# Kernel tuning notes

Hardware: AMD Instinct MI355X
Metric: run time of the kernel (lower is better)

Reference implementation:

```python
import jax, jax.numpy as jnp
import numpy as np

B, S, D, DEPTH = 2, 2048, 1024, 4
NUM_LEAVES = 2 ** DEPTH          # 16
NUM_DEC = NUM_LEAVES - 1         # 15


def setup_inputs() -> dict:
    key = jax.random.key(0)
    k1, k2, k3, k4, k5 = jax.random.split(key, 5)
    scale = 1.0 / np.sqrt(D)
    return {
        "x": jax.random.normal(k1, (B, S, D), dtype=jnp.float32),
        "dec_w": jax.random.normal(k2, (NUM_DEC, D), dtype=jnp.float32) * scale,
        "dec_b": jax.random.normal(k3, (NUM_DEC,), dtype=jnp.float32) * scale,
        "leaf_w": jax.random.normal(k4, (NUM_LEAVES, D, D), dtype=jnp.float32) * scale,  # [leaf, out, in] (torch Linear layout)
        "leaf_b": jax.random.normal(k5, (NUM_LEAVES, D), dtype=jnp.float32) * scale,
    }


def reference(x, dec_w, dec_b, leaf_w, leaf_b):
    num_leaves = leaf_w.shape[0]
    num_dec = num_leaves - 1
    # All decision-node sigmoids in one batched GEMM: [B,S,num_dec]
    dec = jax.nn.sigmoid(jnp.einsum("bsd,nd->bsn", x, dec_w) + dec_b)
    # Faithful to the original: each tree slot is multiplied exactly once by its
    # direct parent's decision (left child: p, right child: 1-p).
    leaf_idx = np.arange(num_dec, 2 * num_leaves - 1)      # slots holding leaf probs
    parent = (leaf_idx - 1) // 2                           # [num_leaves]
    is_left = (leaf_idx % 2 == 1)                          # [num_leaves]
    dec_p = dec[..., parent]                               # [B,S,num_leaves]
    leaf_probs = jnp.where(jnp.asarray(is_left), dec_p, 1.0 - dec_p)
    # All leaf MLPs as one batched GEMM: [B,S,L,D]
    leaf_out = jnp.einsum("bsd,lod->bslo", x, leaf_w) + leaf_b
    # Probability-weighted sum over leaves -> [B,S,D]
    return jnp.einsum("bslo,bsl->bso", leaf_out, leaf_probs)
```

## Files before the change

### kernel.cpp

```cpp
#include <hip/hip_runtime.h>
#include <stdint.h>


#define M_TOK 4096
#define DDIM  1024
#define KFLAT 9216

typedef __bf16 bf16x8 __attribute__((ext_vector_type(8)));
typedef float  f32x4  __attribute__((ext_vector_type(4)));
typedef unsigned short u16x4 __attribute__((ext_vector_type(4)));
typedef unsigned short u16x8 __attribute__((ext_vector_type(8)));

#define GLB(p) ((const __attribute__((address_space(1))) void*)(p))
#define LDS(p) ((__attribute__((address_space(3))) void*)(p))

__device__ __forceinline__ unsigned short f2bf(float f) {
    union { float f; uint32_t u; } v; v.f = f;
    uint32_t u = v.u;
    return (unsigned short)((u + 0x7fffu + ((u >> 16) & 1u)) >> 16);
}

__device__ __forceinline__ bf16x8 asbf(f32x4 v) {
    bf16x8 r; __builtin_memcpy(&r, &v, 16); return r;
}

template<int OFF>
__device__ __forceinline__ f32x4 dsr(uint32_t a) {
    f32x4 r;
    asm volatile("ds_read_b128 %0, %1 offset:%c2" : "=v"(r) : "v"(a), "i"(OFF));
    return r;
}

__global__ __launch_bounds__(256) void prep_dec_kernel(
    const float* __restrict__ x, const float* __restrict__ dec_w,
    const float* __restrict__ dec_b, const float* __restrict__ lw,
    const float* __restrict__ lb, unsigned short* __restrict__ wp,
    float* __restrict__ bw, unsigned short* __restrict__ xs,
    float* __restrict__ pmat, int newlay)
{
    if (blockIdx.x < 1024) {
        int idx = blockIdx.x * 256 + threadIdx.x;
        int o  = idx >> 8;
        int k4 = (idx & 255) << 2;
        size_t src = (size_t)o * DDIM + k4;
        const int nt = o >> 8, wn = (o >> 6) & 3, jj = (o >> 4) & 3, ra = o & 15;
        auto store4 = [&](int l, u16x4 d) {
            if (newlay) {
                int K    = l * DDIM + k4;
                int kt   = K >> 6;
                int half = (K >> 5) & 1;
                int g16  = (K >> 3) & 3;
                int e0   = K & 7;
                size_t a = ((size_t)(nt * 144 + kt) * 4 + wn) * 4096
                         + (jj * 2 + half) * 512 + (g16 * 16 + ra) * 8 + e0;
                *(u16x4*)(wp + a) = d;
            } else {
                *(u16x4*)(wp + (size_t)o * KFLAT + l * DDIM + k4) = d;
            }
        };
        float4 acc = make_float4(0.f, 0.f, 0.f, 0.f);
#pragma unroll
        for (int j = 0; j < 8; ++j) {
            const float4 a = *(const float4*)(lw + (size_t)(2*j)   * DDIM*DDIM + src);
            const float4 b = *(const float4*)(lw + (size_t)(2*j+1) * DDIM*DDIM + src);
            u16x4 d;
            d[0] = f2bf(a.x - b.x); d[1] = f2bf(a.y - b.y);
            d[2] = f2bf(a.z - b.z); d[3] = f2bf(a.w - b.w);
            store4(j, d);
            acc.x += b.x; acc.y += b.y; acc.z += b.z; acc.w += b.w;
        }
        u16x4 s;
        s[0] = f2bf(acc.x); s[1] = f2bf(acc.y); s[2] = f2bf(acc.z); s[3] = f2bf(acc.w);
        store4(8, s);
        if ((idx & 255) == 0) {
            float sb = 0.f;
#pragma unroll
            for (int j = 0; j < 8; ++j) {
                float ba = lb[(2*j) * DDIM + o];
                float bb = lb[(2*j+1) * DDIM + o];
                bw[j * DDIM + o] = ba - bb;
                sb += bb;
            }
            bw[8 * DDIM + o] = sb;
        }
    } else {
        int m    = (blockIdx.x - 1024) * 4 + (threadIdx.x >> 6);
        int lane = threadIdx.x & 63;
        const float* xr = x + (size_t)m * DDIM + lane * 16;
        float xv[16];
        *(float4*)&xv[0]  = *(const float4*)(xr + 0);
        *(float4*)&xv[4]  = *(const float4*)(xr + 4);
        *(float4*)&xv[8]  = *(const float4*)(xr + 8);
        *(float4*)&xv[12] = *(const float4*)(xr + 12);
        float s[8];
#pragma unroll
        for (int j = 0; j < 8; ++j) {
            const float* wr = dec_w + (size_t)(7 + j) * DDIM + lane * 16;
            float a = 0.f;
#pragma unroll
            for (int i = 0; i < 16; i += 4) {
                float4 wv = *(const float4*)(wr + i);
                a = fmaf(xv[i], wv.x, fmaf(xv[i+1], wv.y, fmaf(xv[i+2], wv.z, fmaf(xv[i+3], wv.w, a))));
            }
            s[j] = a;
        }
#pragma unroll
        for (int j = 0; j < 8; ++j)
#pragma unroll
            for (int off = 32; off > 0; off >>= 1)
                s[j] += __shfl_xor(s[j], off);
        float p[8];
#pragma unroll
        for (int j = 0; j < 8; ++j)
            p[j] = 1.0f / (1.0f + expf(-(s[j] + dec_b[7 + j])));
        if (lane == 0) {
#pragma unroll
            for (int j = 0; j < 8; ++j)
                pmat[(size_t)m * 8 + j] = p[j];
        }
#pragma unroll
        for (int j = 0; j < 9; ++j) {
            float pj = (j < 8) ? p[j] : 1.0f;
            unsigned short* dst = xs + (size_t)m * KFLAT + j * DDIM + lane * 16;
#pragma unroll
            for (int c = 0; c < 2; ++c) {
                u16x8 o;
#pragma unroll
                for (int e = 0; e < 8; ++e) o[e] = f2bf(pj * xv[c * 8 + e]);
                *(u16x8*)(dst + c * 8) = o;
            }
        }
    }
}

#define WAITV0 asm volatile("s_waitcnt vmcnt(0)" ::: "memory")
#define BARR   __builtin_amdgcn_s_barrier()
#define LGKM0  do { asm volatile("s_waitcnt lgkmcnt(0)" ::: "memory"); \
                    __builtin_amdgcn_sched_barrier(0); } while(0)
#define LGKM4  do { asm volatile("s_waitcnt lgkmcnt(4)" ::: "memory"); \
                    __builtin_amdgcn_sched_barrier(0); } while(0)
#define WAITV4LG4 do { asm volatile("s_waitcnt vmcnt(4) lgkmcnt(4)" ::: "memory"); \
                       __builtin_amdgcn_sched_barrier(0); } while(0)
#define WAITV0LG4 do { asm volatile("s_waitcnt vmcnt(0) lgkmcnt(4)" ::: "memory"); \
                       __builtin_amdgcn_sched_barrier(0); } while(0)

#define MFMA_Q(q, SET) do { \
    __builtin_amdgcn_s_setprio(1); \
    _Pragma("unroll") \
    for (int mfl = 0; mfl < 2; ++mfl) { \
        _Pragma("unroll") \
        for (int j = 0; j < 4; ++j) { \
            acc[2*(q)+mfl][j] = __builtin_amdgcn_mfma_f32_16x16x32_bf16(asbf(SET[mfl][0]), asbf(bv[j][0]), acc[2*(q)+mfl][j], 0, 0, 0); \
            acc[2*(q)+mfl][j] = __builtin_amdgcn_mfma_f32_16x16x32_bf16(asbf(SET[mfl][1]), asbf(bv[j][1]), acc[2*(q)+mfl][j], 0, 0, 0); \
        } \
    } \
    __builtin_amdgcn_s_setprio(0); \
} while(0)

#define RD_A(SET, q, boff) do { \
    SET[0][0] = dsr<(2*(q)+0)*2048>(bA0 + (boff)); \
    SET[0][1] = dsr<(2*(q)+0)*2048>(bA1 + (boff)); \
    SET[1][0] = dsr<(2*(q)+1)*2048>(bA0 + (boff)); \
    SET[1][1] = dsr<(2*(q)+1)*2048>(bA1 + (boff)); \
} while(0)

__global__ __launch_bounds__(512, 2) void tree_gemm6(
    const unsigned short* __restrict__ xs,
    const unsigned short* __restrict__ wpf,
    float* __restrict__ out, float* __restrict__ parts)
{
    extern __shared__ char smem[];
    const int tid  = threadIdx.x;
    const int lane = tid & 63;
    const int w    = tid >> 6;
    const int wm   = w >> 2, wn = w & 3;
    const int ra   = lane & 15;
    const int g16  = lane >> 4;

    const int flat = blockIdx.x;
    const int xcd  = flat & 7;
    const int idx  = flat >> 3;
    const int cc   = idx >> 4;
    const int mt   = idx & 15;
    const int code = xcd * 2 + cc;
    const int nt   = code >> 2;
    const int g    = code & 3;
    const int m0   = mt * 256, n0 = nt * 256;
    const int k0   = g * 2304;
    const int NT   = 36;

    uint32_t sbase = (uint32_t)(uintptr_t)(__attribute__((address_space(3))) char*)smem;
    const uint32_t colb0 = (uint32_t)((g16 ^ (ra & 7)) << 4);
    const uint32_t colb1 = colb0 ^ 64;
    const uint32_t bA0 = sbase + wm * 16384 + ra * 128 + colb0;
    const uint32_t bA1 = sbase + wm * 16384 + ra * 128 + colb1;

    const int kel = (((lane & 7) ^ (lane >> 3)) & 7) * 8;
    const int rA  = w * 8 + (lane >> 3);

    auto stageA = [&](int buf, int tt, int hh) {
        const unsigned short* s0 = xs + (size_t)(m0 + hh * 128 + rA) * KFLAT + (k0 + tt * 64 + kel);
        char* d0 = smem + buf * 32768 + hh * 16384 + w * 1024;
        __builtin_amdgcn_global_load_lds(GLB(s0), LDS(d0), 16, 0, 0);
        __builtin_amdgcn_global_load_lds(GLB(s0 + (size_t)64 * KFLAT), LDS(d0 + 8192), 16, 0, 0);
    };

    const unsigned short* bsrc = wpf
        + ((size_t)(nt * 144 + g * 36) * 4 + wn) * 4096 + lane * 8;

    f32x4 acc[8][4] = {};
    f32x4 avA[2][2], avB[2][2], bv[4][2];

    stageA(0, 0, 0); stageA(0, 0, 1);
    WAITV0;
    BARR;

    for (int t = 0; t < NT; ++t) {
        const bool on = (t + 1 < NT);
#pragma unroll
        for (int j = 0; j < 4; ++j) {
            bv[j][0] = *(const f32x4*)(bsrc + (j * 2 + 0) * 512);
            bv[j][1] = *(const f32x4*)(bsrc + (j * 2 + 1) * 512);
        }
        if (on) { stageA((t + 1) & 1, t + 1, 0); stageA((t + 1) & 1, t + 1, 1); }

        const uint32_t boff = (uint32_t)(t & 1) << 15;
        RD_A(avA, 0, boff);
        RD_A(avB, 1, boff);
        if (on) { WAITV4LG4; } else { WAITV0LG4; }
        MFMA_Q(0, avA);
        RD_A(avA, 2, boff);
        LGKM4;  MFMA_Q(1, avB);
        RD_A(avB, 3, boff);
        LGKM4;  MFMA_Q(2, avA);
        LGKM0;  MFMA_Q(3, avB);

        if (on) { WAITV0; BARR; }
        bsrc += 16384;
    }

    float* dst = (g == 0) ? out : parts + (size_t)(g - 1) * M_TOK * DDIM;
#pragma unroll
    for (int mf = 0; mf < 8; ++mf)
#pragma unroll
        for (int e = 0; e < 4; ++e) {
            int row = m0 + wm * 128 + mf * 16 + g16 * 4 + e;
#pragma unroll
            for (int j = 0; j < 4; ++j)
                dst[(size_t)row * DDIM + n0 + wn * 64 + j * 16 + ra] = acc[mf][j][e];
        }
}

__global__ __launch_bounds__(256) void reduce2_kernel(
    float* __restrict__ out, const float* __restrict__ parts,
    const float* __restrict__ pmat, const float* __restrict__ bw, int np)
{
    size_t i = (size_t)blockIdx.x * 256 + threadIdx.x;
    int m   = (int)(i >> 8);
    int col = (int)(i & 255) * 4;
    float4 a = ((const float4*)out)[i];
    for (int p = 0; p < np; ++p) {
        float4 b = ((const float4*)(parts + (size_t)p * M_TOK * DDIM))[i];
        a.x += b.x; a.y += b.y; a.z += b.z; a.w += b.w;
    }
    float4 pa = *(const float4*)(pmat + (size_t)m * 8);
    float4 pb = *(const float4*)(pmat + (size_t)m * 8 + 4);
    float4 bias = *(const float4*)(bw + 8 * DDIM + col);
#pragma unroll
    for (int l = 0; l < 8; ++l) {
        float pl = (l < 4) ? ((const float*)&pa)[l] : ((const float*)&pb)[l - 4];
        float4 bl = *(const float4*)(bw + l * DDIM + col);
        bias.x = fmaf(pl, bl.x, bias.x); bias.y = fmaf(pl, bl.y, bias.y);
        bias.z = fmaf(pl, bl.z, bias.z); bias.w = fmaf(pl, bl.w, bias.w);
    }
    a.x += bias.x; a.y += bias.y; a.z += bias.z; a.w += bias.w;
    ((float4*)out)[i] = a;
}

#define READ_A5(SET, q) do { \
    SET[0][0] = dsr<(2*(q)+0)*2048>(bA0); \
    SET[0][1] = dsr<(2*(q)+0)*2048>(bA1); \
    SET[1][0] = dsr<(2*(q)+1)*2048>(bA0); \
    SET[1][1] = dsr<(2*(q)+1)*2048>(bA1); \
} while(0)
#define READ_B5() do { \
    bv[0][0] = dsr<0*2048>(bB0); bv[0][1] = dsr<0*2048>(bB1); \
    bv[1][0] = dsr<1*2048>(bB0); bv[1][1] = dsr<1*2048>(bB1); \
    bv[2][0] = dsr<2*2048>(bB0); bv[2][1] = dsr<2*2048>(bB1); \
    bv[3][0] = dsr<3*2048>(bB0); bv[3][1] = dsr<3*2048>(bB1); \
} while(0)
#define WAITV8 asm volatile("s_waitcnt vmcnt(8)" ::: "memory")
#define WAITV4 asm volatile("s_waitcnt vmcnt(4)" ::: "memory")

__global__ __launch_bounds__(512, 2) void tree_gemm5(
    const unsigned short* __restrict__ xs, const unsigned short* __restrict__ wp,
    float* __restrict__ out, float* __restrict__ parts, int KG)
{
    extern __shared__ char smem[];
    const int tid  = threadIdx.x;
    const int lane = tid & 63;
    const int w    = tid >> 6;
    const int wm   = w >> 2, wn = w & 3;
    const int ra   = lane & 15;
    const int g16  = lane >> 4;
    const int bx  = blockIdx.x;
    const int xcd = bx & 7, ii = bx >> 3;
    const int nt  = xcd >> 1;
    const int mt  = (xcd & 1) * 8 + ii;
    const int m0  = mt * 256, n0 = nt * 256;
    const int g   = blockIdx.y;
    const int k0  = g * KG;
    const int NT  = KG >> 6;
    uint32_t sbase = (uint32_t)(uintptr_t)(__attribute__((address_space(3))) char*)smem;
    const uint32_t colb0 = (uint32_t)((g16 ^ (ra & 7)) << 4);
    const uint32_t colb1 = colb0 ^ 64;
    const uint32_t baseA0s = sbase + wm * 16384 + ra * 128 + colb0;
    const uint32_t baseA1s = sbase + wm * 16384 + ra * 128 + colb1;
    const uint32_t baseB0s = sbase + 65536 + wn * 8192 + ra * 128 + colb0;
    const uint32_t baseB1s = sbase + 65536 + wn * 8192 + ra * 128 + colb1;
    const int kel = (((lane & 7) ^ (lane >> 3)) & 7) * 8;
    const int rA  = w * 8 + (lane >> 3);
    auto stageA = [&](int buf, int tt, int hh) {
        const unsigned short* s0 = xs + (size_t)(m0 + hh * 128 + rA) * KFLAT + (k0 + tt * 64 + kel);
        char* d0 = smem + buf * 32768 + hh * 16384 + w * 1024;
        __builtin_amdgcn_global_load_lds(GLB(s0), LDS(d0), 16, 0, 0);
        __builtin_amdgcn_global_load_lds(GLB(s0 + (size_t)64 * KFLAT), LDS(d0 + 8192), 16, 0, 0);
    };
    auto stageB = [&](int buf, int tt, int hh) {
        const unsigned short* s0 = wp + (size_t)(n0 + hh * 128 + rA) * KFLAT + (k0 + tt * 64 + kel);
        char* d0 = smem + 65536 + buf * 32768 + hh * 16384 + w * 1024;
        __builtin_amdgcn_global_load_lds(GLB(s0), LDS(d0), 16, 0, 0);
        __builtin_amdgcn_global_load_lds(GLB(s0 + (size_t)64 * KFLAT), LDS(d0 + 8192), 16, 0, 0);
    };
    f32x4 acc[8][4] = {};
    f32x4 avA[2][2], avB[2][2], bv[4][2];
    stageA(0, 0, 0); stageA(0, 0, 1);
    stageB(0, 0, 0); stageB(0, 0, 1);
    stageA(1, 1, 0); stageA(1, 1, 1);
    stageB(1, 1, 0); stageB(1, 1, 1);
    WAITV8; BARR;
    int bt = 0, bt2 = 2;
    for (int t = 0; t < NT; ++t) {
        if (t) {
            if (t == NT - 1) { WAITV0; } else { WAITV4; }
            BARR;
        }
        if (t + 1 < NT) { stageA((t + 1) & 1, t + 1, 0); stageA((t + 1) & 1, t + 1, 1); }
        if (t + 2 < NT) { stageB(bt2, t + 2, 0); stageB(bt2, t + 2, 1); }
        const uint32_t aoff = (uint32_t)(t & 1) << 15;
        const uint32_t boffv = (uint32_t)bt << 15;
        const uint32_t bA0 = baseA0s + aoff, bA1 = baseA1s + aoff;
        const uint32_t bB0 = baseB0s + boffv, bB1 = baseB1s + boffv;
        READ_B5();
        READ_A5(avA, 0);
        READ_A5(avB, 1);
        LGKM4;  MFMA_Q(0, avA);
        READ_A5(avA, 2);
        LGKM4;  MFMA_Q(1, avB);
        READ_A5(avB, 3);
        LGKM4;  MFMA_Q(2, avA);
        LGKM0;  MFMA_Q(3, avB);
        bt  = (bt  == 2) ? 0 : bt  + 1;
        bt2 = (bt2 == 2) ? 0 : bt2 + 1;
    }
    float* dst = (g == 0) ? out : parts + (size_t)(g - 1) * M_TOK * DDIM;
#pragma unroll
    for (int mf = 0; mf < 8; ++mf)
#pragma unroll
        for (int e = 0; e < 4; ++e) {
            int row = m0 + wm * 128 + mf * 16 + g16 * 4 + e;
#pragma unroll
            for (int j = 0; j < 4; ++j)
                dst[(size_t)row * DDIM + n0 + wn * 64 + j * 16 + ra] = acc[mf][j][e];
        }
}

__global__ __launch_bounds__(256, 4) void tree_gemm3(
    const unsigned short* __restrict__ xs, const unsigned short* __restrict__ wp,
    const float* __restrict__ bw, const float* __restrict__ pmat,
    float* __restrict__ out, float* __restrict__ parts, int KG)
{
    __shared__ __align__(16) unsigned short Asm[2][128 * 32];
    __shared__ __align__(16) unsigned short Bsm[2][128 * 32];
    const int tid  = threadIdx.x;
    const int lane = tid & 63;
    const int w    = tid >> 6;
    const int wm   = w >> 1, wn = w & 1;
    const int bx   = blockIdx.x;
    const int xcd  = bx & 7;
    const int ii   = bx >> 3;
    const int mt   = xcd * 4 + (ii >> 3);
    const int nt   = ii & 7;
    const int m0   = mt * 128, n0 = nt * 128;
    const int g    = blockIdx.y;
    const int k0   = g * KG;
    const int ra   = lane & 15;
    const int kb   = (lane >> 4) * 8;
    f32x4 acc[4][4] = {};
    auto stage = [&](int buf, int t) {
#pragma unroll
        for (int c = 0; c < 2; ++c) {
            int row = w * 32 + c * 16 + (lane >> 2);
            int ke  = k0 + t * 32 + (lane & 3) * 8;
            const unsigned short* ga = xs + (size_t)(m0 + row) * KFLAT + ke;
            __builtin_amdgcn_global_load_lds(GLB(ga), LDS(&Asm[buf][w * 1024 + c * 512]), 16, 0, 0);
            const unsigned short* gb = wp + (size_t)(n0 + row) * KFLAT + ke;
            __builtin_amdgcn_global_load_lds(GLB(gb), LDS(&Bsm[buf][w * 1024 + c * 512]), 16, 0, 0);
        }
    };
    const int TOT = KG >> 5;
    stage(0, 0);
    __syncthreads();
    int cur = 0;
    for (int t = 0; t < TOT; ++t) {
        if (t + 1 < TOT) stage(cur ^ 1, t + 1);
        bf16x8 av2[4], bv2[4];
#pragma unroll
        for (int i2 = 0; i2 < 4; ++i2)
            av2[i2] = *(const bf16x8*)&Asm[cur][(wm * 64 + i2 * 16 + ra) * 32 + kb];
#pragma unroll
        for (int j = 0; j < 4; ++j)
            bv2[j] = *(const bf16x8*)&Bsm[cur][(wn * 64 + j * 16 + ra) * 32 + kb];
#pragma unroll
        for (int i2 = 0; i2 < 4; ++i2)
#pragma unroll
            for (int j = 0; j < 4; ++j)
                acc[i2][j] = __builtin_amdgcn_mfma_f32_16x16x32_bf16(av2[i2], bv2[j], acc[i2][j], 0, 0, 0);
        __syncthreads();
        cur ^= 1;
    }
    float* bsm = (float*)&Asm[0][0];
    if (g == 0) {
        for (int idx = tid; idx < 9 * 128; idx += 256)
            bsm[idx] = bw[(idx >> 7) * DDIM + n0 + (idx & 127)];
    }
    __syncthreads();
    float* dst = (g == 0) ? out : parts + (size_t)(g - 1) * M_TOK * DDIM;
#pragma unroll
    for (int i2 = 0; i2 < 4; ++i2)
#pragma unroll
        for (int r = 0; r < 4; ++r) {
            int row = m0 + wm * 64 + i2 * 16 + (lane >> 4) * 4 + r;
            float4 pa, pb;
            if (g == 0) {
                pa = *(const float4*)(pmat + (size_t)row * 8);
                pb = *(const float4*)(pmat + (size_t)row * 8 + 4);
            }
#pragma unroll
            for (int j = 0; j < 4; ++j) {
                int cl = wn * 64 + j * 16 + ra;
                float v = acc[i2][j][r];
                if (g == 0) {
                    v += pa.x * bsm[0 * 128 + cl] + pa.y * bsm[1 * 128 + cl]
                       + pa.z * bsm[2 * 128 + cl] + pa.w * bsm[3 * 128 + cl]
                       + pb.x * bsm[4 * 128 + cl] + pb.y * bsm[5 * 128 + cl]
                       + pb.z * bsm[6 * 128 + cl] + pb.w * bsm[7 * 128 + cl]
                       + bsm[8 * 128 + cl];
                }
                dst[(size_t)row * DDIM + n0 + cl] = v;
            }
        }
}

__global__ __launch_bounds__(256) void reduce_kernel(
    float* __restrict__ out, const float* __restrict__ parts, int np)
{
    size_t i = (size_t)blockIdx.x * 256 + threadIdx.x;
    float4 a = ((const float4*)out)[i];
    for (int p = 0; p < np; ++p) {
        float4 b = ((const float4*)(parts + (size_t)p * M_TOK * DDIM))[i];
        a.x += b.x; a.y += b.y; a.z += b.z; a.w += b.w;
    }
    ((float4*)out)[i] = a;
}

extern "C" void kernel_launch(void* const* d_in, const int* in_sizes, int n_in,
                              void* d_out, int out_size, void* d_ws, size_t ws_size,
                              hipStream_t stream) {
    (void)in_sizes; (void)n_in; (void)out_size;
    const float* x     = (const float*)d_in[0];
    const float* dec_w = (const float*)d_in[1];
    const float* dec_b = (const float*)d_in[2];
    const float* lw    = (const float*)d_in[3];
    const float* lb    = (const float*)d_in[4];
    float* out = (float*)d_out;
    uint8_t* w8 = (uint8_t*)d_ws;

    unsigned short* xs   = (unsigned short*)(w8);
    unsigned short* wp   = (unsigned short*)(w8 + 75497472);
    float*          bw   = (float*)(w8 + 94371840);
    float*          pmat = (float*)(w8 + 94408704);
    float*          parts= (float*)(w8 + 94539776);
    const size_t NEED3 = 94539776 + 2ull * 16777216;
    const size_t NEED4 = 94539776 + 3ull * 16777216;

    int ks = (ws_size >= NEED4) ? 4 : (ws_size >= NEED3) ? 3 : 0;
    if (!ks) return;

    bool use6 = false;
    if (ks == 4) {
        hipError_t e6 = hipFuncSetAttribute(
            reinterpret_cast<const void*>(tree_gemm6),
            hipFuncAttributeMaxDynamicSharedMemorySize, 65536);
        use6 = (e6 == hipSuccess);
    }

    prep_dec_kernel<<<2048, 256, 0, stream>>>(x, dec_w, dec_b, lw, lb, wp, bw, xs, pmat,
                                              use6 ? 1 : 0);

    if (use6) {
        tree_gemm6<<<256, 512, 65536, stream>>>(xs, wp, out, parts);
        reduce2_kernel<<<4096, 256, 0, stream>>>(out, parts, pmat, bw, 3);
        return;
    }

    hipError_t e5 = hipFuncSetAttribute(
        reinterpret_cast<const void*>(tree_gemm5),
        hipFuncAttributeMaxDynamicSharedMemorySize, 163840);
    if (e5 == hipSuccess) {
        tree_gemm5<<<dim3(64, ks), 512, 163840, stream>>>(xs, wp, out, parts, KFLAT / ks);
        reduce2_kernel<<<4096, 256, 0, stream>>>(out, parts, pmat, bw, ks - 1);
    } else {
        tree_gemm3<<<dim3(256, ks), 256, 0, stream>>>(xs, wp, bw, pmat, out, parts, KFLAT / ks);
        reduce_kernel<<<4096, 256, 0, stream>>>(out, parts, ks - 1);
    }
}
```

Before: 141.8 us.

## Replace register-streamed B GEMM with smaller 128x256 tile LDS-staged kernel

Swaps the tree_gemm6 path, which streamed pre-swizzled weight fragments straight from global memory into registers, for a new tree_gemm7 kernel. The new kernel stages both A and B through LDS with global_load_lds, double-buffered over k-steps of 32, using 128x256 tiles and a 512-block grid with four blocks per CU. The weight prep now writes a plain row-major layout again instead of the MFMA-fragment layout. The aim is higher occupancy and better latency hiding, at the cost of less reuse per tile, twice the k-iterations, and a barrier on every step.

```diff
diff --git a/kernel.cpp b/kernel.cpp
--- a/kernel.cpp
+++ b/kernel.cpp
@@ -36,28 +36,14 @@
     const float* __restrict__ dec_b, const float* __restrict__ lw,
     const float* __restrict__ lb, unsigned short* __restrict__ wp,
     float* __restrict__ bw, unsigned short* __restrict__ xs,
-    float* __restrict__ pmat, int newlay)
+    float* __restrict__ pmat)
 {
     if (blockIdx.x < 1024) {
         int idx = blockIdx.x * 256 + threadIdx.x;
         int o  = idx >> 8;
         int k4 = (idx & 255) << 2;
         size_t src = (size_t)o * DDIM + k4;
-        const int nt = o >> 8, wn = (o >> 6) & 3, jj = (o >> 4) & 3, ra = o & 15;
-        auto store4 = [&](int l, u16x4 d) {
-            if (newlay) {
-                int K    = l * DDIM + k4;
-                int kt   = K >> 6;
-                int half = (K >> 5) & 1;
-                int g16  = (K >> 3) & 3;
-                int e0   = K & 7;
-                size_t a = ((size_t)(nt * 144 + kt) * 4 + wn) * 4096
-                         + (jj * 2 + half) * 512 + (g16 * 16 + ra) * 8 + e0;
-                *(u16x4*)(wp + a) = d;
-            } else {
-                *(u16x4*)(wp + (size_t)o * KFLAT + l * DDIM + k4) = d;
-            }
-        };
+        size_t dstb = (size_t)o * KFLAT + k4;
         float4 acc = make_float4(0.f, 0.f, 0.f, 0.f);
 #pragma unroll
         for (int j = 0; j < 8; ++j) {
@@ -66,12 +52,12 @@
             u16x4 d;
             d[0] = f2bf(a.x - b.x); d[1] = f2bf(a.y - b.y);
             d[2] = f2bf(a.z - b.z); d[3] = f2bf(a.w - b.w);
-            store4(j, d);
+            *(u16x4*)(wp + dstb + (size_t)j * DDIM) = d;
             acc.x += b.x; acc.y += b.y; acc.z += b.z; acc.w += b.w;
         }
         u16x4 s;
         s[0] = f2bf(acc.x); s[1] = f2bf(acc.y); s[2] = f2bf(acc.z); s[3] = f2bf(acc.w);
-        store4(8, s);
+        *(u16x4*)(wp + dstb + (size_t)8 * DDIM) = s;
         if ((idx & 255) == 0) {
             float sb = 0.f;
 #pragma unroll
@@ -134,15 +120,145 @@
 }
 
 #define WAITV0 asm volatile("s_waitcnt vmcnt(0)" ::: "memory")
+#define WAITV4 asm volatile("s_waitcnt vmcnt(4)" ::: "memory")
+#define WAITV8 asm volatile("s_waitcnt vmcnt(8)" ::: "memory")
 #define BARR   __builtin_amdgcn_s_barrier()
 #define LGKM0  do { asm volatile("s_waitcnt lgkmcnt(0)" ::: "memory"); \
                     __builtin_amdgcn_sched_barrier(0); } while(0)
+#define LGKM2  do { asm volatile("s_waitcnt lgkmcnt(2)" ::: "memory"); \
+                    __builtin_amdgcn_sched_barrier(0); } while(0)
 #define LGKM4  do { asm volatile("s_waitcnt lgkmcnt(4)" ::: "memory"); \
                     __builtin_amdgcn_sched_barrier(0); } while(0)
-#define WAITV4LG4 do { asm volatile("s_waitcnt vmcnt(4) lgkmcnt(4)" ::: "memory"); \
-                       __builtin_amdgcn_sched_barrier(0); } while(0)
-#define WAITV0LG4 do { asm volatile("s_waitcnt vmcnt(0) lgkmcnt(4)" ::: "memory"); \
-                       __builtin_amdgcn_sched_barrier(0); } while(0)
+
+__global__ __launch_bounds__(512, 4) void tree_gemm7(
+    const unsigned short* __restrict__ xs,
+    const unsigned short* __restrict__ wp,
+    float* __restrict__ out, float* __restrict__ parts)
+{
+    extern __shared__ char smem[];
+    const int tid  = threadIdx.x;
+    const int lane = tid & 63;
+    const int w    = tid >> 6;
+    const int wm   = w >> 2, wn = w & 3;
+    const int ra   = lane & 15;
+    const int g16  = lane >> 4;
+
+    const int bx   = blockIdx.x;
+    const int xcd  = bx & 7;
+    const int rest = bx >> 3;
+    const int cc   = rest >> 5;
+    const int mt   = rest & 31;
+    const int code = xcd * 2 + cc;
+    const int nt   = code >> 2;
+    const int g    = code & 3;
+    const int m0   = mt * 128, n0 = nt * 256;
+    const int k0   = g * 2304;
+    const int NT   = 72;
+
+    uint32_t sbase = (uint32_t)(uintptr_t)(__attribute__((address_space(3))) char*)smem;
+    const uint32_t colb = (uint32_t)((g16 ^ ((ra >> 1) & 3)) << 4);
+    const uint32_t bAr = sbase + (uint32_t)(wm * 64 + ra) * 64 + colb;
+    const uint32_t bBr = sbase + 16384 + (uint32_t)(wn * 64 + ra) * 64 + colb;
+
+    const int rowS = tid >> 2;
+    const int kel  = (((tid & 3) ^ ((tid >> 3) & 3)) & 3) * 8;
+
+    auto stageA = [&](int buf, int tt) {
+        const unsigned short* s0 = xs + (size_t)(m0 + rowS) * KFLAT + (k0 + tt * 32 + kel);
+        char* d0 = smem + buf * 8192 + w * 1024;
+        __builtin_amdgcn_global_load_lds(GLB(s0), LDS(d0), 16, 0, 0);
+    };
+    auto stageB = [&](int buf, int tt) {
+        const unsigned short* s0 = wp + (size_t)(n0 + rowS) * KFLAT + (k0 + tt * 32 + kel);
+        char* d0 = smem + 16384 + buf * 16384 + w * 1024;
+        __builtin_amdgcn_global_load_lds(GLB(s0), LDS(d0), 16, 0, 0);
+        __builtin_amdgcn_global_load_lds(GLB(s0 + (size_t)128 * KFLAT), LDS(d0 + 8192), 16, 0, 0);
+    };
+
+    f32x4 acc[4][4] = {};
+    f32x4 av[4], bv[4];
+
+    stageA(0, 0); stageB(0, 0);
+    WAITV0;
+    BARR;
+
+    for (int t = 0; t < NT; ++t) {
+        const bool on = (t + 1 < NT);
+        if (on) { stageA((t + 1) & 1, t + 1); stageB((t + 1) & 1, t + 1); }
+
+        const uint32_t bA = bAr + ((uint32_t)(t & 1) << 13);
+        const uint32_t bB = bBr + ((uint32_t)(t & 1) << 14);
+        av[0] = dsr<0>(bA);    av[1] = dsr<1024>(bA);
+        bv[0] = dsr<0>(bB);    bv[1] = dsr<1024>(bB);
+        bv[2] = dsr<2048>(bB); bv[3] = dsr<3072>(bB);
+        av[2] = dsr<2048>(bA); av[3] = dsr<3072>(bA);
+
+        LGKM4;
+        __builtin_amdgcn_s_setprio(1);
+#pragma unroll
+        for (int m = 0; m < 2; ++m)
+#pragma unroll
+            for (int j = 0; j < 2; ++j)
+                acc[m][j] = __builtin_amdgcn_mfma_f32_16x16x32_bf16(asbf(av[m]), asbf(bv[j]), acc[m][j], 0, 0, 0);
+        __builtin_amdgcn_s_setprio(0);
+        LGKM2;
+        __builtin_amdgcn_s_setprio(1);
+#pragma unroll
+        for (int m = 0; m < 2; ++m)
+#pragma unroll
+            for (int j = 2; j < 4; ++j)
+                acc[m][j] = __builtin_amdgcn_mfma_f32_16x16x32_bf16(asbf(av[m]), asbf(bv[j]), acc[m][j], 0, 0, 0);
+        __builtin_amdgcn_s_setprio(0);
+        LGKM0;
+        __builtin_amdgcn_s_setprio(1);
+#pragma unroll
+        for (int m = 2; m < 4; ++m)
+#pragma unroll
+            for (int j = 0; j < 4; ++j)
+                acc[m][j] = __builtin_amdgcn_mfma_f32_16x16x32_bf16(asbf(av[m]), asbf(bv[j]), acc[m][j], 0, 0, 0);
+        __builtin_amdgcn_s_setprio(0);
+
+        WAITV0;
+        BARR;
+    }
+
+    float* dst = (g == 0) ? out : parts + (size_t)(g - 1) * M_TOK * DDIM;
+#pragma unroll
+    for (int m = 0; m < 4; ++m)
+#pragma unroll
+        for (int e = 0; e < 4; ++e) {
+            int row = m0 + wm * 64 + m * 16 + g16 * 4 + e;
+#pragma unroll
+            for (int j = 0; j < 4; ++j)
+                dst[(size_t)row * DDIM + n0 + wn * 64 + j * 16 + ra] = acc[m][j][e];
+        }
+}
+
+__global__ __launch_bounds__(256) void reduce2_kernel(
+    float* __restrict__ out, const float* __restrict__ parts,
+    const float* __restrict__ pmat, const float* __restrict__ bw, int np)
+{
+    size_t i = (size_t)blockIdx.x * 256 + threadIdx.x;
+    int m   = (int)(i >> 8);
+    int col = (int)(i & 255) * 4;
+    float4 a = ((const float4*)out)[i];
+    for (int p = 0; p < np; ++p) {
+        float4 b = ((const float4*)(parts + (size_t)p * M_TOK * DDIM))[i];
+        a.x += b.x; a.y += b.y; a.z += b.z; a.w += b.w;
+    }
+    float4 pa = *(const float4*)(pmat + (size_t)m * 8);
+    float4 pb = *(const float4*)(pmat + (size_t)m * 8 + 4);
+    float4 bias = *(const float4*)(bw + 8 * DDIM + col);
+#pragma unroll
+    for (int l = 0; l < 8; ++l) {
+        float pl = (l < 4) ? ((const float*)&pa)[l] : ((const float*)&pb)[l - 4];
+        float4 bl = *(const float4*)(bw + l * DDIM + col);
+        bias.x = fmaf(pl, bl.x, bias.x); bias.y = fmaf(pl, bl.y, bias.y);
+        bias.z = fmaf(pl, bl.z, bias.z); bias.w = fmaf(pl, bl.w, bias.w);
+    }
+    a.x += bias.x; a.y += bias.y; a.z += bias.z; a.w += bias.w;
+    ((float4*)out)[i] = a;
+}
 
 #define MFMA_Q(q, SET) do { \
     __builtin_amdgcn_s_setprio(1); \
@@ -156,127 +272,6 @@
     } \
     __builtin_amdgcn_s_setprio(0); \
 } while(0)
-
-#define RD_A(SET, q, boff) do { \
-    SET[0][0] = dsr<(2*(q)+0)*2048>(bA0 + (boff)); \
-    SET[0][1] = dsr<(2*(q)+0)*2048>(bA1 + (boff)); \
-    SET[1][0] = dsr<(2*(q)+1)*2048>(bA0 + (boff)); \
-    SET[1][1] = dsr<(2*(q)+1)*2048>(bA1 + (boff)); \
-} while(0)
-
-__global__ __launch_bounds__(512, 2) void tree_gemm6(
-    const unsigned short* __restrict__ xs,
-    const unsigned short* __restrict__ wpf,
-    float* __restrict__ out, float* __restrict__ parts)
-{
-    extern __shared__ char smem[];
-    const int tid  = threadIdx.x;
-    const int lane = tid & 63;
-    const int w    = tid >> 6;
-    const int wm   = w >> 2, wn = w & 3;
-    const int ra   = lane & 15;
-    const int g16  = lane >> 4;
-
-    const int flat = blockIdx.x;
-    const int xcd  = flat & 7;
-    const int idx  = flat >> 3;
-    const int cc   = idx >> 4;
-    const int mt   = idx & 15;
-    const int code = xcd * 2 + cc;
-    const int nt   = code >> 2;
-    const int g    = code & 3;
-    const int m0   = mt * 256, n0 = nt * 256;
-    const int k0   = g * 2304;
-    const int NT   = 36;
-
-    uint32_t sbase = (uint32_t)(uintptr_t)(__attribute__((address_space(3))) char*)smem;
-    const uint32_t colb0 = (uint32_t)((g16 ^ (ra & 7)) << 4);
-    const uint32_t colb1 = colb0 ^ 64;
-    const uint32_t bA0 = sbase + wm * 16384 + ra * 128 + colb0;
-    const uint32_t bA1 = sbase + wm * 16384 + ra * 128 + colb1;
-
-    const int kel = (((lane & 7) ^ (lane >> 3)) & 7) * 8;
-    const int rA  = w * 8 + (lane >> 3);
-
-    auto stageA = [&](int buf, int tt, int hh) {
-        const unsigned short* s0 = xs + (size_t)(m0 + hh * 128 + rA) * KFLAT + (k0 + tt * 64 + kel);
-        char* d0 = smem + buf * 32768 + hh * 16384 + w * 1024;
-        __builtin_amdgcn_global_load_lds(GLB(s0), LDS(d0), 16, 0, 0);
-        __builtin_amdgcn_global_load_lds(GLB(s0 + (size_t)64 * KFLAT), LDS(d0 + 8192), 16, 0, 0);
-    };
-
-    const unsigned short* bsrc = wpf
-        + ((size_t)(nt * 144 + g * 36) * 4 + wn) * 4096 + lane * 8;
-
-    f32x4 acc[8][4] = {};
-    f32x4 avA[2][2], avB[2][2], bv[4][2];
-
-    stageA(0, 0, 0); stageA(0, 0, 1);
-    WAITV0;
-    BARR;
-
-    for (int t = 0; t < NT; ++t) {
-        const bool on = (t + 1 < NT);
-#pragma unroll
-        for (int j = 0; j < 4; ++j) {
-            bv[j][0] = *(const f32x4*)(bsrc + (j * 2 + 0) * 512);
-            bv[j][1] = *(const f32x4*)(bsrc + (j * 2 + 1) * 512);
-        }
-        if (on) { stageA((t + 1) & 1, t + 1, 0); stageA((t + 1) & 1, t + 1, 1); }
-
-        const uint32_t boff = (uint32_t)(t & 1) << 15;
-        RD_A(avA, 0, boff);
-        RD_A(avB, 1, boff);
-        if (on) { WAITV4LG4; } else { WAITV0LG4; }
-        MFMA_Q(0, avA);
-        RD_A(avA, 2, boff);
-        LGKM4;  MFMA_Q(1, avB);
-        RD_A(avB, 3, boff);
-        LGKM4;  MFMA_Q(2, avA);
-        LGKM0;  MFMA_Q(3, avB);
-
-        if (on) { WAITV0; BARR; }
-        bsrc += 16384;
-    }
-
-    float* dst = (g == 0) ? out : parts + (size_t)(g - 1) * M_TOK * DDIM;
-#pragma unroll
-    for (int mf = 0; mf < 8; ++mf)
-#pragma unroll
-        for (int e = 0; e < 4; ++e) {
-            int row = m0 + wm * 128 + mf * 16 + g16 * 4 + e;
-#pragma unroll
-            for (int j = 0; j < 4; ++j)
-                dst[(size_t)row * DDIM + n0 + wn * 64 + j * 16 + ra] = acc[mf][j][e];
-        }
-}
-
-__global__ __launch_bounds__(256) void reduce2_kernel(
-    float* __restrict__ out, const float* __restrict__ parts,
-    const float* __restrict__ pmat, const float* __restrict__ bw, int np)
-{
-    size_t i = (size_t)blockIdx.x * 256 + threadIdx.x;
-    int m   = (int)(i >> 8);
-    int col = (int)(i & 255) * 4;
-    float4 a = ((const float4*)out)[i];
-    for (int p = 0; p < np; ++p) {
-        float4 b = ((const float4*)(parts + (size_t)p * M_TOK * DDIM))[i];
-        a.x += b.x; a.y += b.y; a.z += b.z; a.w += b.w;
-    }
-    float4 pa = *(const float4*)(pmat + (size_t)m * 8);
-    float4 pb = *(const float4*)(pmat + (size_t)m * 8 + 4);
-    float4 bias = *(const float4*)(bw + 8 * DDIM + col);
-#pragma unroll
-    for (int l = 0; l < 8; ++l) {
-        float pl = (l < 4) ? ((const float*)&pa)[l] : ((const float*)&pb)[l - 4];
-        float4 bl = *(const float4*)(bw + l * DDIM + col);
-        bias.x = fmaf(pl, bl.x, bias.x); bias.y = fmaf(pl, bl.y, bias.y);
-        bias.z = fmaf(pl, bl.z, bias.z); bias.w = fmaf(pl, bl.w, bias.w);
-    }
-    a.x += bias.x; a.y += bias.y; a.z += bias.z; a.w += bias.w;
-    ((float4*)out)[i] = a;
-}
-
 #define READ_A5(SET, q) do { \
     SET[0][0] = dsr<(2*(q)+0)*2048>(bA0); \
     SET[0][1] = dsr<(2*(q)+0)*2048>(bA1); \
@@ -289,8 +284,6 @@
     bv[2][0] = dsr<2*2048>(bB0); bv[2][1] = dsr<2*2048>(bB1); \
     bv[3][0] = dsr<3*2048>(bB0); bv[3][1] = dsr<3*2048>(bB1); \
 } while(0)
-#define WAITV8 asm volatile("s_waitcnt vmcnt(8)" ::: "memory")
-#define WAITV4 asm volatile("s_waitcnt vmcnt(4)" ::: "memory")
 
 __global__ __launch_bounds__(512, 2) void tree_gemm5(
     const unsigned short* __restrict__ xs, const unsigned short* __restrict__ wp,
@@ -497,21 +490,17 @@
     int ks = (ws_size >= NEED4) ? 4 : (ws_size >= NEED3) ? 3 : 0;
     if (!ks) return;
 
-    bool use6 = false;
+    prep_dec_kernel<<<2048, 256, 0, stream>>>(x, dec_w, dec_b, lw, lb, wp, bw, xs, pmat);
+
     if (ks == 4) {
-        hipError_t e6 = hipFuncSetAttribute(
-            reinterpret_cast<const void*>(tree_gemm6),
-            hipFuncAttributeMaxDynamicSharedMemorySize, 65536);
-        use6 = (e6 == hipSuccess);
-    }
-
-    prep_dec_kernel<<<2048, 256, 0, stream>>>(x, dec_w, dec_b, lw, lb, wp, bw, xs, pmat,
-                                              use6 ? 1 : 0);
-
-    if (use6) {
-        tree_gemm6<<<256, 512, 65536, stream>>>(xs, wp, out, parts);
-        reduce2_kernel<<<4096, 256, 0, stream>>>(out, parts, pmat, bw, 3);
-        return;
+        hipError_t e7 = hipFuncSetAttribute(
+            reinterpret_cast<const void*>(tree_gemm7),
+            hipFuncAttributeMaxDynamicSharedMemorySize, 49152);
+        if (e7 == hipSuccess) {
+            tree_gemm7<<<512, 512, 49152, stream>>>(xs, wp, out, parts);
+            reduce2_kernel<<<4096, 256, 0, stream>>>(out, parts, pmat, bw, 3);
+            return;
+        }
     }
 
     hipError_t e5 = hipFuncSetAttribute(
```

Result: no change. 139.1 us (-1.9%).
